# Kernel optimization log

Measured on AMD Instinct MI355X. Metric: run time of the kernel, lower is better.

## Reference

```python
import jax, jax.numpy as jnp
import numpy as np

PERIODS = (7, 30, 90)
KEEP_ORIGINAL = True
DROP_NA = False
T, F = 262144, 64


def setup_inputs() -> dict:
    key = jax.random.key(0)
    x = jax.random.normal(key, (T, F), dtype=jnp.float32)
    return {"x": x}


def _moving_average(x, cumsum, period):
    # drop_na=False path of _compute_ma:
    #   i <  period-1 : cumsum[i] / (i+1)   (i==0 gives x[0], same as cumsum[0]/1)
    #   i >= period-1 : (cumsum[i] - cumsum[i-period]) / period, with cumsum[i-period]=0 at i==period-1
    t = x.shape[0]
    idx = jnp.arange(t)
    shifted = jnp.concatenate(
        [jnp.zeros((period,) + x.shape[1:], dtype=x.dtype), cumsum[:-period]], axis=0
    )
    windowed = (cumsum - shifted) / jnp.asarray(period, x.dtype)
    expanding = cumsum / (idx + 1).astype(x.dtype)[:, None]
    return jnp.where((idx >= period - 1)[:, None], windowed, expanding)


def reference(x):
    cumsum = jnp.cumsum(x, axis=0)  # shared prefix sum across all periods
    parts = [x] if KEEP_ORIGINAL else []
    for p in PERIODS:
        parts.append(_moving_average(x, cumsum, p))
    # drop_na=False -> all parts have length T, min_batch_size = T
    return jnp.concatenate(parts, axis=-1)  # [T, (1+len(PERIODS))*F]
```

## Files before the change

### kernel.cpp

```cpp
#include <hip/hip_runtime.h>


#define T_ROWS 262144
#define F_COLS 64
#define OUT_COLS 256
#define CHUNK 128
#define CHUNKS_PER_BLOCK 4

__global__ __launch_bounds__(256) void ma_kernel(const float* __restrict__ x,
                                                 float* __restrict__ out) {
    const int tid   = threadIdx.x;
    const int col   = tid & 63;
    const int chunk = blockIdx.x * CHUNKS_PER_BLOCK + (tid >> 6);
    const long r0   = (long)chunk * CHUNK;

    const float* __restrict__ xc = x + col;
    float* __restrict__ oc = out + col;

    float s7 = 0.f, s30 = 0.f, s90 = 0.f;

    if (chunk == 0) {
        for (int i = 0; i < CHUNK; ++i) {
            float v = xc[(long)i * F_COLS];
            s7 += v; s30 += v; s90 += v;
            if (i >= 7)  s7  -= xc[(long)(i - 7)  * F_COLS];
            if (i >= 30) s30 -= xc[(long)(i - 30) * F_COLS];
            if (i >= 90) s90 -= xc[(long)(i - 90) * F_COLS];
            float d7  = (i < 6)  ? (float)(i + 1) : 7.f;
            float d30 = (i < 29) ? (float)(i + 1) : 30.f;
            float d90 = (i < 89) ? (float)(i + 1) : 90.f;
            long ob = (long)i * OUT_COLS;
            oc[ob]       = v;
            oc[ob + 64]  = s7  / d7;
            oc[ob + 128] = s30 / d30;
            oc[ob + 192] = s90 / d90;
        }
    } else {
        #pragma unroll
        for (int k = 1; k <= 7; ++k) {
            float v = xc[(r0 - k) * F_COLS];
            s7 += v; s30 += v; s90 += v;
        }
        #pragma unroll
        for (int k = 8; k <= 30; ++k) {
            float v = xc[(r0 - k) * F_COLS];
            s30 += v; s90 += v;
        }
        #pragma unroll 2
        for (int k = 31; k <= 90; ++k) {
            s90 += xc[(r0 - k) * F_COLS];
        }

        const float r7 = 1.f / 7.f, r30 = 1.f / 30.f, r90 = 1.f / 90.f;
        #pragma unroll 4
        for (int i = 0; i < CHUNK; ++i) {
            const long gi = r0 + i;
            float v   = xc[gi * F_COLS];
            float o7  = xc[(gi - 7)  * F_COLS];
            float o30 = xc[(gi - 30) * F_COLS];
            float o90 = xc[(gi - 90) * F_COLS];
            s7  += v - o7;
            s30 += v - o30;
            s90 += v - o90;
            const long ob = gi * OUT_COLS;
            oc[ob]       = v;
            oc[ob + 64]  = s7  * r7;
            oc[ob + 128] = s30 * r30;
            oc[ob + 192] = s90 * r90;
        }
    }
}

extern "C" void kernel_launch(void* const* d_in, const int* in_sizes, int n_in,
                              void* d_out, int out_size, void* d_ws, size_t ws_size,
                              hipStream_t stream) {
    const float* x = (const float*)d_in[0];
    float* out = (float*)d_out;
    const int n_chunks = T_ROWS / CHUNK;
    const int n_blocks = n_chunks / CHUNKS_PER_BLOCK;
    ma_kernel<<<n_blocks, 256, 0, stream>>>(x, out);
}
```

Measured before the change: 368.5 us.

## Stage input tile plus halo in LDS and split rows into strips per thread

Each block now loads a 128-row tile plus a 90-row halo of x into shared memory with float4 loads, then 8 strips of 16 rows each compute sliding sums from LDS. This replaces the repeated global loads of lagged rows (four per output row plus a 90-row warmup per thread) with LDS reads, and raises parallelism by giving each thread fewer rows. The cost is per-block halo redundancy (218 rows loaded for 128 produced), a longer 90-element warmup relative to the 16-row strip, and about 56KB of LDS per block, which limits occupancy.

```diff
diff --git a/kernel.cpp b/kernel.cpp
--- a/kernel.cpp
+++ b/kernel.cpp
@@ -4,69 +4,92 @@
 #define T_ROWS 262144
 #define F_COLS 64
 #define OUT_COLS 256
-#define CHUNK 128
-#define CHUNKS_PER_BLOCK 4
+#define TILE 128
+#define HALO 90
+#define STAGE_ROWS (TILE + HALO)
+#define THREADS 512
+#define STRIPS 8
+#define STRIP_ROWS (TILE / STRIPS)
 
-__global__ __launch_bounds__(256) void ma_kernel(const float* __restrict__ x,
-                                                 float* __restrict__ out) {
-    const int tid   = threadIdx.x;
+__global__ __launch_bounds__(THREADS) void ma_kernel(const float* __restrict__ x,
+                                                     float* __restrict__ out) {
+    __shared__ float lds[STAGE_ROWS * F_COLS];
+
+    const int tid = threadIdx.x;
+    const long base = (long)blockIdx.x * TILE;
+
+    {
+        const long g0f = (base - HALO) * F_COLS;
+        float4* lds4 = (float4*)lds;
+        const int n4 = STAGE_ROWS * F_COLS / 4;
+        if (base >= HALO) {
+            const float4* __restrict__ src = (const float4*)(x + g0f);
+            for (int idx = tid; idx < n4; idx += THREADS)
+                lds4[idx] = src[idx];
+        } else {
+            for (int idx = tid; idx < n4; idx += THREADS) {
+                long gf = g0f + (long)idx * 4;
+                float4 v = make_float4(0.f, 0.f, 0.f, 0.f);
+                if (gf >= 0) v = *(const float4*)(x + gf);
+                lds4[idx] = v;
+            }
+        }
+    }
+    __syncthreads();
+
     const int col   = tid & 63;
-    const int chunk = blockIdx.x * CHUNKS_PER_BLOCK + (tid >> 6);
-    const long r0   = (long)chunk * CHUNK;
+    const int strip = tid >> 6;
+    const int lr0   = HALO + strip * STRIP_ROWS;
+    const long g0   = base + strip * STRIP_ROWS;
 
-    const float* __restrict__ xc = x + col;
+    const float* __restrict__ lc = lds + col;
+
+    float s7 = 0.f, s30 = 0.f, s90 = 0.f;
+    #pragma unroll
+    for (int k = 1; k <= 7; ++k)  s7  += lc[(lr0 - k) * F_COLS];
+    s30 = s7;
+    #pragma unroll
+    for (int k = 8; k <= 30; ++k) s30 += lc[(lr0 - k) * F_COLS];
+    s90 = s30;
+    #pragma unroll
+    for (int k = 31; k <= 90; ++k) s90 += lc[(lr0 - k) * F_COLS];
+
     float* __restrict__ oc = out + col;
 
-    float s7 = 0.f, s30 = 0.f, s90 = 0.f;
-
-    if (chunk == 0) {
-        for (int i = 0; i < CHUNK; ++i) {
-            float v = xc[(long)i * F_COLS];
-            s7 += v; s30 += v; s90 += v;
-            if (i >= 7)  s7  -= xc[(long)(i - 7)  * F_COLS];
-            if (i >= 30) s30 -= xc[(long)(i - 30) * F_COLS];
-            if (i >= 90) s90 -= xc[(long)(i - 90) * F_COLS];
-            float d7  = (i < 6)  ? (float)(i + 1) : 7.f;
-            float d30 = (i < 29) ? (float)(i + 1) : 30.f;
-            float d90 = (i < 89) ? (float)(i + 1) : 90.f;
-            long ob = (long)i * OUT_COLS;
-            oc[ob]       = v;
-            oc[ob + 64]  = s7  / d7;
-            oc[ob + 128] = s30 / d30;
-            oc[ob + 192] = s90 / d90;
+    if (g0 < 89) {
+        for (int j = 0; j < STRIP_ROWS; ++j) {
+            const int lr = lr0 + j;
+            const long gi = g0 + j;
+            float v   = lc[lr * F_COLS];
+            float o7  = lc[(lr - 7)  * F_COLS];
+            float o30 = lc[(lr - 30) * F_COLS];
+            float o90 = lc[(lr - 90) * F_COLS];
+            s7 += v - o7; s30 += v - o30; s90 += v - o90;
+            float fi  = (float)(gi + 1);
+            float d7  = (gi < 6)  ? fi : 7.f;
+            float d30 = (gi < 29) ? fi : 30.f;
+            float d90 = (gi < 89) ? fi : 90.f;
+            float* o = oc + gi * OUT_COLS;
+            o[0]   = v;
+            o[64]  = s7  / d7;
+            o[128] = s30 / d30;
+            o[192] = s90 / d90;
         }
     } else {
+        const float r7 = 1.f / 7.f, r30 = 1.f / 30.f, r90 = 1.f / 90.f;
         #pragma unroll
-        for (int k = 1; k <= 7; ++k) {
-            float v = xc[(r0 - k) * F_COLS];
-            s7 += v; s30 += v; s90 += v;
-        }
-        #pragma unroll
-        for (int k = 8; k <= 30; ++k) {
-            float v = xc[(r0 - k) * F_COLS];
-            s30 += v; s90 += v;
-        }
-        #pragma unroll 2
-        for (int k = 31; k <= 90; ++k) {
-            s90 += xc[(r0 - k) * F_COLS];
-        }
-
-        const float r7 = 1.f / 7.f, r30 = 1.f / 30.f, r90 = 1.f / 90.f;
-        #pragma unroll 4
-        for (int i = 0; i < CHUNK; ++i) {
-            const long gi = r0 + i;
-            float v   = xc[gi * F_COLS];
-            float o7  = xc[(gi - 7)  * F_COLS];
-            float o30 = xc[(gi - 30) * F_COLS];
-            float o90 = xc[(gi - 90) * F_COLS];
-            s7  += v - o7;
-            s30 += v - o30;
-            s90 += v - o90;
-            const long ob = gi * OUT_COLS;
-            oc[ob]       = v;
-            oc[ob + 64]  = s7  * r7;
-            oc[ob + 128] = s30 * r30;
-            oc[ob + 192] = s90 * r90;
+        for (int j = 0; j < STRIP_ROWS; ++j) {
+            const int lr = lr0 + j;
+            float v   = lc[lr * F_COLS];
+            float o7  = lc[(lr - 7)  * F_COLS];
+            float o30 = lc[(lr - 30) * F_COLS];
+            float o90 = lc[(lr - 90) * F_COLS];
+            s7 += v - o7; s30 += v - o30; s90 += v - o90;
+            float* o = oc + (g0 + j) * OUT_COLS;
+            o[0]   = v;
+            o[64]  = s7  * r7;
+            o[128] = s30 * r30;
+            o[192] = s90 * r90;
         }
     }
 }
@@ -76,7 +99,6 @@
                               hipStream_t stream) {
     const float* x = (const float*)d_in[0];
     float* out = (float*)d_out;
-    const int n_chunks = T_ROWS / CHUNK;
-    const int n_blocks = n_chunks / CHUNKS_PER_BLOCK;
-    ma_kernel<<<n_blocks, 256, 0, stream>>>(x, out);
+    const int n_blocks = T_ROWS / TILE;
+    ma_kernel<<<n_blocks, THREADS, 0, stream>>>(x, out);
 }
```

New measurement: 312.7 us. 15.1% less time.
